# Performance work log

Hardware: AMD Instinct MI355X
Metric: run time of the kernel (lower is better)

Reference implementation:

```python
import jax, jax.numpy as jnp
import numpy as np

BETA = 0.9
THRESHOLD = 1.0  # snntorch Leaky default threshold, reset_mechanism='subtract'
ALPHA = 2.0      # snntorch default ATan surrogate alpha (irrelevant for fwd)


def spike_fn(x):
    # Heaviside spike: fires when membrane exceeds threshold (x = mem - threshold)
    return (x > 0).astype(x.dtype)


def setup_inputs() -> dict:
    key = jax.random.key(0)
    k1, k2, k3 = jax.random.split(key, 3)
    T, B, NIN, HID = 1024, 128, 256, 1024
    # Bernoulli spike train input (the module consumes spikes)
    spike_seq = (jax.random.uniform(k1, (T, B, NIN)) < 0.2).astype(jnp.float32)
    # Xavier-uniform-ish init for fc1, scaled for fc2 (gain=0.5)
    lim1 = float(np.sqrt(6.0 / (NIN + HID)))
    W1 = jax.random.uniform(k2, (HID, NIN), minval=-lim1, maxval=lim1, dtype=jnp.float32)
    b1 = jnp.zeros((HID,), jnp.float32)
    lim2 = 0.5 * float(np.sqrt(6.0 / (HID + 2)))
    W2 = jax.random.uniform(k3, (2, HID), minval=-lim2, maxval=lim2, dtype=jnp.float32)
    # avoidance bias: +0.8 on first/second half columns (as in _init_weights)
    half = NIN // 2
    W2 = W2.at[1, :half].add(0.8)
    W2 = W2.at[0, half:NIN].add(0.8)
    b2 = jnp.zeros((2,), jnp.float32)
    return {"spike_seq": spike_seq, "W1": W1, "b1": b1, "W2": W2, "b2": b2}


def reference(spike_seq, W1, b1, W2, b2):
    T, B, _ = spike_seq.shape
    HID = W1.shape[0]
    mem1_0 = jnp.zeros((B, HID), spike_seq.dtype)
    mem2_0 = jnp.zeros((B, 2), spike_seq.dtype)

    def step(carry, x_t):
        mem1, mem2 = carry
        h = x_t @ W1.T + b1                      # [B, HID]
        mem1 = BETA * mem1 + h
        spk1 = spike_fn(mem1 - THRESHOLD)
        mem1 = mem1 - spk1 * THRESHOLD           # subtract reset
        h2 = spk1 @ W2.T + b2                    # [B, 2]
        mem2 = BETA * mem2 + h2
        spk2 = spike_fn(mem2 - THRESHOLD)
        mem2 = mem2 - spk2 * THRESHOLD
        return (mem1, mem2), (spk2, spk1)

    (mem1_f, mem2_f), (out_spikes, hidden_spikes) = jax.lax.scan(
        step, (mem1_0, mem2_0), spike_seq)
    return out_spikes, hidden_spikes, mem2_f
```

## Files before the change

### kernel.cpp

```cpp
#include <hip/hip_runtime.h>
#include <hip/hip_bf16.h>
#include <stdint.h>


#define TT  1024
#define BB  128
#define NIN 256
#define HID 1024

#define OFF_HID  262144ULL
#define OFF_MEM2 134479872ULL

typedef float f4 __attribute__((ext_vector_type(4)));

__global__ __launch_bounds__(256) void k_transpose(const float* __restrict__ W1,
                                                   float* __restrict__ W1T) {
    int idx = blockIdx.x * 256 + threadIdx.x;
    if (idx >= 257 * 1024) return;
    int j = idx & (HID - 1);
    int i = idx >> 10;
    W1T[(size_t)i * HID + j] = (i < NIN) ? W1[(size_t)j * NIN + i] : 0.0f;
}

__global__ __launch_bounds__(256) void k_pack(const float* __restrict__ x,
                                              unsigned int* __restrict__ cntArr,
                                              unsigned char* __restrict__ idxArr,
                                              int slots) {
    size_t tb = blockIdx.x;
    int tid = threadIdx.x;
    int lane = tid & 63, w = tid >> 6;
    float v = x[tb * NIN + tid];
    bool act = v > 0.5f;
    unsigned long long m = __ballot(act);
    __shared__ unsigned int wc[4];
    __shared__ unsigned char sIdx[96];
    if (lane == 0) wc[w] = (unsigned int)__popcll(m);
    __syncthreads();
    unsigned int off = 0;
#pragma unroll
    for (int k = 0; k < 4; ++k) if (k < w) off += wc[k];
    unsigned int cnt = wc[0] + wc[1] + wc[2] + wc[3];
    unsigned int rank = off + (unsigned int)__popcll(m & ((1ull << lane) - 1));
    if (act && rank < (unsigned int)slots) sIdx[rank] = (unsigned char)tid;
    __syncthreads();
    if (tid * 4 < slots)
        ((unsigned int*)(idxArr + tb * (size_t)slots))[tid] = ((const unsigned int*)sIdx)[tid];
    if (tid == 0) cntArr[tb] = cnt;
}

__global__ __launch_bounds__(256, 2) void k_snn(const float* __restrict__ W1T,
                                                const unsigned int* __restrict__ cntArr,
                                                const unsigned char* __restrict__ idxArr,
                                                const float* __restrict__ x,
                                                const float* __restrict__ b1,
                                                float* __restrict__ outHid,
                                                int slots) {
#pragma clang fp contract(off)
    const int jc   = blockIdx.x & 15;
    const int bg   = blockIdx.x >> 4;
    const int tid  = threadIdx.x;
    const int lane = tid & 63;
    const int wave = tid >> 6;
    const int b    = (bg << 2) + wave;
    const int q    = lane & 15;
    const int s    = lane >> 4;
    const int jq   = (jc << 6) + (q << 2);
    const int jq4  = jq >> 2;

    __shared__ f4 sW4[257 * 16];
    __shared__ f4 sEx[4][64];

    for (int p = tid; p < NIN * 16; p += 256) {
        int i = p >> 4, qq = p & 15;
        sW4[p] = *reinterpret_cast<const f4*>(W1T + (size_t)i * HID + (jc << 6) + (qq << 2));
    }
    if (tid < 16) { f4 z; z.x = 0.f; z.y = 0.f; z.z = 0.f; z.w = 0.f; sW4[256 * 16 + tid] = z; }
    __syncthreads();

    f4 mem4;
    mem4.x = 0.f; mem4.y = 0.f; mem4.z = 0.f; mem4.w = 0.f;
    const f4 bs = *reinterpret_cast<const f4*>(b1 + jq);
    const int ub = __builtin_amdgcn_readfirstlane(b);
    const int sl = slots;
    const int dwTot = sl >> 2;
    int dwA = q;            if (dwA >= dwTot) dwA = dwTot - 1;
    int dwB = 16 + (q & 7); if (dwB >= dwTot) dwB = dwTot - 1;

    const bool sLo   = (s < 2);
    const bool sEven = ((s & 1) == 0);
    const f4* __restrict__ W1Tf4 = reinterpret_cast<const f4*>(W1T);

    unsigned offCnt = (unsigned)((s * BB + ub) * 4);
    unsigned offA   = (unsigned)((s * BB + ub) * sl + dwA * 4);
    unsigned offB   = (unsigned)((s * BB + ub) * sl + dwB * 4);
    const unsigned stC = (unsigned)(4 * BB * 4);
    const unsigned stL = (unsigned)(4 * BB * sl);

    unsigned cnt_v = *(const unsigned*)((const char*)cntArr + offCnt);
    unsigned vA_v  = *(const unsigned*)(idxArr + offA);
    unsigned vB_v  = *(const unsigned*)(idxArr + offB);

    float* outP = outHid + ((size_t)s * BB + b) * HID + jq;
    const size_t outStep = (size_t)4 * BB * HID;

#define RL(v, l) ((unsigned)__builtin_amdgcn_readlane((int)(v), (l)))
#define FETCH_D(kd, dOut) do {                                                  \
        unsigned _d0, _d1, _d2, _d3;                                            \
        if ((kd) < 16) {                                                        \
            _d0 = RL(vA, (kd));      _d1 = RL(vA, 16 + (kd));                   \
            _d2 = RL(vA, 32 + (kd)); _d3 = RL(vA, 48 + (kd));                   \
        } else { int _m = (kd) - 16;                                            \
            _d0 = RL(vB, _m);        _d1 = RL(vB, 16 + _m);                     \
            _d2 = RL(vB, 32 + _m);   _d3 = RL(vB, 48 + _m); }                   \
        unsigned _dl = sEven ? _d0 : _d1;                                       \
        unsigned _dh = sEven ? _d2 : _d3;                                       \
        dOut = sLo ? _dl : _dh;                                                 \
    } while (0)

#define FETCH_A(kd, dOut) do {                                                  \
        unsigned _d0 = RL(vA, (kd));      unsigned _d1 = RL(vA, 16 + (kd));     \
        unsigned _d2 = RL(vA, 32 + (kd)); unsigned _d3 = RL(vA, 48 + (kd));     \
        unsigned _dl = sEven ? _d0 : _d1;                                       \
        unsigned _dh = sEven ? _d2 : _d3;                                       \
        dOut = sLo ? _dl : _dh;                                                 \
    } while (0)

#define B_LDS(kd, PRED) do {                                                    \
        unsigned d_; FETCH_A(kd, d_);                                           \
        int kb_ = (kd) << 2;                                                    \
        _Pragma("unroll")                                                       \
        for (int i2 = 0; i2 < 4; ++i2) {                                        \
            unsigned row_ = (d_ >> (8 * i2)) & 255u;                            \
            if (PRED) row_ = ((unsigned)(kb_ + i2) < mylim) ? row_ : 256u;      \
            h4 += sW4[row_ * 16 + q];               \
        }                                                                       \
    } while (0)

#define WISS(n) do {                                                            \
        if (isu < dwEnd) {                                                      \
            unsigned d_; FETCH_D(isu, d_);                                      \
            unsigned r0_ = d_ & 255u, r1_ = (d_ >> 8) & 255u;                   \
            unsigned r2_ = (d_ >> 16) & 255u, r3_ = d_ >> 24;                   \
            if (isu >= predFrom) {                                              \
                int kb_ = isu << 2;                                             \
                r0_ = ((unsigned)(kb_    ) < mylim) ? r0_ : 256u;               \
                r1_ = ((unsigned)(kb_ + 1) < mylim) ? r1_ : 256u;               \
                r2_ = ((unsigned)(kb_ + 2) < mylim) ? r2_ : 256u;               \
                r3_ = ((unsigned)(kb_ + 3) < mylim) ? r3_ : 256u;               \
            }                                                                   \
            w##n##a = W1Tf4[(r0_ << 8) + jq4];                                  \
            w##n##b = W1Tf4[(r1_ << 8) + jq4];                                  \
            w##n##c = W1Tf4[(r2_ << 8) + jq4];                                  \
            w##n##d = W1Tf4[(r3_ << 8) + jq4];                                  \
            ++isu;                                                              \
        }                                                                       \
    } while (0)

#define WCON(n) do { h4 += w##n##a; h4 += w##n##b; h4 += w##n##c; h4 += w##n##d; } while (0)

    const int SPLIT = 9;

    for (int t = 0; t < TT; t += 4) {
        unsigned cnt = cnt_v, vA = vA_v, vB = vB_v;

        unsigned st = (t + 4 < TT) ? 1u : 0u;
        offCnt += st * stC; offA += st * stL; offB += st * stL;
        cnt_v = *(const unsigned*)((const char*)cntArr + offCnt);
        vA_v  = *(const unsigned*)(idxArr + offA);
        vB_v  = *(const unsigned*)(idxArr + offB);

        unsigned mylim = cnt < (unsigned)sl ? cnt : (unsigned)sl;
        int l0 = __builtin_amdgcn_readlane((int)mylim, 0);
        int l1 = __builtin_amdgcn_readlane((int)mylim, 16);
        int l2 = __builtin_amdgcn_readlane((int)mylim, 32);
        int l3 = __builtin_amdgcn_readlane((int)mylim, 48);
        int kmax = l0 > l1 ? l0 : l1; kmax = kmax > l2 ? kmax : l2; kmax = kmax > l3 ? kmax : l3;
        int kmin = l0 < l1 ? l0 : l1; kmin = kmin < l2 ? kmin : l2; kmin = kmin < l3 ? kmin : l3;

        int dwEnd = (kmax + 3) >> 2;
        int dwL   = dwEnd < SPLIT ? dwEnd : SPLIT;
        int dwLm  = (kmin >> 2) < dwL ? (kmin >> 2) : dwL;
        int predFrom = kmin >> 2;

        f4 e0, e1, e2, e3;

        if (!__any((int)(cnt > (unsigned)sl))) {
            f4 h4 = bs;

            f4 w0a, w0b, w0c, w0d;
            f4 w1a, w1b, w1c, w1d;
            f4 w2a, w2b, w2c, w2d;
            f4 w3a, w3b, w3c, w3d;
            int isu = SPLIT;
            WISS(0); WISS(1); WISS(2); WISS(3);

            int kd = 0;
            for (; kd < dwLm; ++kd) B_LDS(kd, false);
            for (; kd < dwL;  ++kd) B_LDS(kd, true);

            int kc = SPLIT;
            for (; kc + 4 <= dwEnd; kc += 4) {
                WCON(0); WISS(0);
                WCON(1); WISS(1);
                WCON(2); WISS(2);
                WCON(3); WISS(3);
            }
            int rem = dwEnd - kc;
            if (rem > 0) WCON(0);
            if (rem > 1) WCON(1);
            if (rem > 2) WCON(2);

            sEx[wave][lane] = h4;
            e0 = sEx[wave][q];
            e1 = sEx[wave][16 + q];
            e2 = sEx[wave][32 + q];
            e3 = sEx[wave][48 + q];
        } else {
#pragma unroll
            for (int tt = 0; tt < 4; ++tt) {
                const float* xr = x + ((size_t)(t + tt) * BB + ub) * NIN;
                f4 g = bs;
                for (int w2 = 0; w2 < 4; ++w2) {
                    unsigned long long m = __ballot(xr[(w2 << 6) + lane] > 0.5f);
                    while (m) {
                        int i = (w2 << 6) + __builtin_ctzll(m);
                        m &= m - 1;
                        g += sW4[i * 16 + q];
                    }
                }
                if      (tt == 0) e0 = g;
                else if (tt == 1) e1 = g;
                else if (tt == 2) e2 = g;
                else              e3 = g;
            }
        }

#define MSTEP4(ev, so0, so1, so2, so3) {                                        \
        f4 mm_ = 0.9f * mem4; mm_ = mm_ + (ev);                                 \
        so0 = (mm_.x - 1.0f > 0.0f) ? 1.0f : 0.0f;                              \
        so1 = (mm_.y - 1.0f > 0.0f) ? 1.0f : 0.0f;                              \
        so2 = (mm_.z - 1.0f > 0.0f) ? 1.0f : 0.0f;                              \
        so3 = (mm_.w - 1.0f > 0.0f) ? 1.0f : 0.0f;                              \
        f4 sp_; sp_.x = so0; sp_.y = so1; sp_.z = so2; sp_.w = so3;             \
        mem4 = mm_ - sp_;                                                       \
    }
        float sA0, sA1, sA2, sA3, sB0, sB1, sB2, sB3;
        float sC0, sC1, sC2, sC3, sD0, sD1, sD2, sD3;
        MSTEP4(e0, sA0, sA1, sA2, sA3)
        MSTEP4(e1, sB0, sB1, sB2, sB3)
        MSTEP4(e2, sC0, sC1, sC2, sC3)
        MSTEP4(e3, sD0, sD1, sD2, sD3)
#undef MSTEP4

        f4 sv;
        sv.x = sLo ? (sEven ? sA0 : sB0) : (sEven ? sC0 : sD0);
        sv.y = sLo ? (sEven ? sA1 : sB1) : (sEven ? sC1 : sD1);
        sv.z = sLo ? (sEven ? sA2 : sB2) : (sEven ? sC2 : sD2);
        sv.w = sLo ? (sEven ? sA3 : sB3) : (sEven ? sC3 : sD3);
        *reinterpret_cast<f4*>(outP) = sv;
        outP += outStep;
    }
#undef WCON
#undef WISS
#undef B_LDS
#undef FETCH_A
#undef FETCH_D
#undef RL
}

__global__ __launch_bounds__(256) void k_h2(const float* __restrict__ spk,
                                            const float* __restrict__ W2,
                                            const float* __restrict__ b2,
                                            float* __restrict__ h2) {
#pragma clang fp contract(off)
    const int lane = threadIdx.x & 63;
    const int wave = threadIdx.x >> 6;
    size_t tb = (size_t)blockIdx.x * 4 + wave;
    const float* row = spk + tb * HID;
    float s0 = 0.0f, s1 = 0.0f;
#pragma unroll
    for (int c = 0; c < 16; ++c) {
        float v  = row[c * 64 + lane];
        float r0 = v * W2[c * 64 + lane];
        float r1 = v * W2[HID + c * 64 + lane];
#pragma unroll
        for (int off = 32; off > 0; off >>= 1) {
            r0 += __shfl_xor(r0, off, 64);
            r1 += __shfl_xor(r1, off, 64);
        }
        s0 += r0;
        s1 += r1;
    }
    s0 += b2[0];
    s1 += b2[1];
    if (lane == 0)
        *reinterpret_cast<float2*>(h2 + tb * 2) = make_float2(s0, s1);
}

__global__ __launch_bounds__(256) void k_scan(const float* __restrict__ h2,
                                              float* __restrict__ outSpk,
                                              float* __restrict__ outMem2) {
#pragma clang fp contract(off)
    const int tid = threadIdx.x;
    float mem = 0.0f;
    float cur[8], nxt[8];
#pragma unroll
    for (int k = 0; k < 8; ++k) cur[k] = h2[k * 256 + tid];
    for (int t0 = 0; t0 < TT; t0 += 8) {
#pragma unroll
        for (int k = 0; k < 8; ++k) {
            int tn = t0 + 8 + k;
            nxt[k] = (tn < TT) ? h2[tn * 256 + tid] : 0.0f;
        }
#pragma unroll
        for (int k = 0; k < 8; ++k) {
            float mm = 0.9f * mem;
            mm = mm + cur[k];
            float spk = (mm - 1.0f > 0.0f) ? 1.0f : 0.0f;
            mm = mm - spk;
            mem = mm;
            outSpk[(t0 + k) * 256 + tid] = spk;
        }
#pragma unroll
        for (int k = 0; k < 8; ++k) cur[k] = nxt[k];
    }
    outMem2[tid] = mem;
}

extern "C" void kernel_launch(void* const* d_in, const int* in_sizes, int n_in,
                              void* d_out, int out_size, void* d_ws, size_t ws_size,
                              hipStream_t stream) {
    const float* x  = (const float*)d_in[0];
    const float* W1 = (const float*)d_in[1];
    const float* b1 = (const float*)d_in[2];
    const float* W2 = (const float*)d_in[3];
    const float* b2 = (const float*)d_in[4];
    float* out = (float*)d_out;

    char* ws = (char*)d_ws;
    float*         W1T = (float*)(ws);
    unsigned int*  cnt = (unsigned int*)(ws + (2 << 20));
    unsigned char* idx = (unsigned char*)(ws + (2 << 20) + (1 << 19));

    size_t fixedB = (size_t)(2 << 20) + (1 << 19) + (1 << 20);
    size_t avail  = ws_size > fixedB ? ws_size - fixedB : 0;
    long   s      = (long)((avail / 131072) & ~(size_t)7);
    int slots = (int)(s > 96 ? 96 : (s < 8 ? 8 : s));

    float* h2 = (float*)(ws + (2 << 20) + (1 << 19) + (size_t)131072 * (size_t)slots);

    k_transpose<<<1028, 256, 0, stream>>>(W1, W1T);
    k_pack<<<131072, 256, 0, stream>>>(x, cnt, idx, slots);
    k_snn<<<512, 256, 0, stream>>>(W1T, cnt, idx, x, b1, out + OFF_HID, slots);
    k_h2<<<32768, 256, 0, stream>>>(out + OFF_HID, W2, b2, h2);
    k_scan<<<1, 256, 0, stream>>>(h2, out, out + OFF_MEM2);
}
```

Before: 1.202 ms.

## Split input rows between LDS and global W1T, narrow column tile to raise occupancy

Only the first 152 input rows of the W1T column slice are kept in LDS. Active inputs above that split are now read straight from global memory, so k_pack builds separate low and high index lists of 48 slots each, with both counts packed into one word. Each block covers 32 columns instead of 64 and each wave handles 8 timesteps per iteration instead of 4. The smaller LDS footprint allows launch bounds of 4 blocks per CU and twice as many blocks. The trade is more global W1T traffic and more readlane and select work per step in exchange for higher occupancy. It also assumes a fixed 16MB index region and no longer sizes slots from ws_size.

```diff
diff --git a/kernel.cpp b/kernel.cpp
--- a/kernel.cpp
+++ b/kernel.cpp
@@ -7,6 +7,7 @@
 #define BB  128
 #define NIN 256
 #define HID 1024
+#define SPLITR 152
 
 #define OFF_HID  262144ULL
 #define OFF_MEM2 134479872ULL
@@ -23,131 +24,118 @@
 }
 
 __global__ __launch_bounds__(256) void k_pack(const float* __restrict__ x,
-                                              unsigned int* __restrict__ cntArr,
-                                              unsigned char* __restrict__ idxArr,
-                                              int slots) {
+                                              unsigned* __restrict__ cntArr,
+                                              unsigned char* __restrict__ idxArr) {
     size_t tb = blockIdx.x;
-    int tid = threadIdx.x;
-    int lane = tid & 63, w = tid >> 6;
+    int tid = threadIdx.x, lane = tid & 63, w = tid >> 6;
     float v = x[tb * NIN + tid];
-    bool act = v > 0.5f;
-    unsigned long long m = __ballot(act);
-    __shared__ unsigned int wc[4];
+    bool act  = v > 0.5f;
+    bool isLo = tid < SPLITR;
+    unsigned long long mLo = __ballot(act && isLo);
+    unsigned long long mHi = __ballot(act && !isLo);
+    __shared__ unsigned wcLo[4], wcHi[4];
     __shared__ unsigned char sIdx[96];
-    if (lane == 0) wc[w] = (unsigned int)__popcll(m);
+    if (lane == 0) { wcLo[w] = (unsigned)__popcll(mLo); wcHi[w] = (unsigned)__popcll(mHi); }
     __syncthreads();
-    unsigned int off = 0;
-#pragma unroll
-    for (int k = 0; k < 4; ++k) if (k < w) off += wc[k];
-    unsigned int cnt = wc[0] + wc[1] + wc[2] + wc[3];
-    unsigned int rank = off + (unsigned int)__popcll(m & ((1ull << lane) - 1));
-    if (act && rank < (unsigned int)slots) sIdx[rank] = (unsigned char)tid;
+    unsigned offLo = 0, offHi = 0;
+#pragma unroll
+    for (int k = 0; k < 4; ++k) if (k < w) { offLo += wcLo[k]; offHi += wcHi[k]; }
+    unsigned cntLo = wcLo[0] + wcLo[1] + wcLo[2] + wcLo[3];
+    unsigned cntHi = wcHi[0] + wcHi[1] + wcHi[2] + wcHi[3];
+    unsigned long long below = (1ull << lane) - 1;
+    unsigned rLo = offLo + (unsigned)__popcll(mLo & below);
+    unsigned rHi = offHi + (unsigned)__popcll(mHi & below);
+    if (act && isLo  && rLo < 48) sIdx[rLo]      = (unsigned char)tid;
+    if (act && !isLo && rHi < 48) sIdx[48 + rHi] = (unsigned char)tid;
     __syncthreads();
-    if (tid * 4 < slots)
-        ((unsigned int*)(idxArr + tb * (size_t)slots))[tid] = ((const unsigned int*)sIdx)[tid];
-    if (tid == 0) cntArr[tb] = cnt;
-}
-
-__global__ __launch_bounds__(256, 2) void k_snn(const float* __restrict__ W1T,
-                                                const unsigned int* __restrict__ cntArr,
+    if (tid < 24) ((unsigned*)(idxArr + tb * 128))[tid] = ((const unsigned*)sIdx)[tid];
+    if (tid == 0) cntArr[tb] = cntLo | (cntHi << 16);
+}
+
+__global__ __launch_bounds__(256, 4) void k_snn(const float* __restrict__ W1T,
+                                                const unsigned* __restrict__ cntArr,
                                                 const unsigned char* __restrict__ idxArr,
                                                 const float* __restrict__ x,
                                                 const float* __restrict__ b1,
-                                                float* __restrict__ outHid,
-                                                int slots) {
+                                                float* __restrict__ outHid) {
 #pragma clang fp contract(off)
-    const int jc   = blockIdx.x & 15;
-    const int bg   = blockIdx.x >> 4;
+    const int jc   = blockIdx.x & 31;
+    const int bg   = blockIdx.x >> 5;
     const int tid  = threadIdx.x;
     const int lane = tid & 63;
     const int wave = tid >> 6;
     const int b    = (bg << 2) + wave;
-    const int q    = lane & 15;
-    const int s    = lane >> 4;
-    const int jq   = (jc << 6) + (q << 2);
-    const int jq4  = jq >> 2;
-
-    __shared__ f4 sW4[257 * 16];
+    const int q    = lane & 7;
+    const int s    = lane >> 3;
+    const int jq   = (jc << 5) + (q << 2);
+    const int jq4  = (jc << 3) + q;
+    const bool sb0 = (s & 1) != 0, sb1 = (s & 2) != 0, sb2 = (s & 4) != 0;
+
+    __shared__ f4 sW4[153 * 8];
     __shared__ f4 sEx[4][64];
-
-    for (int p = tid; p < NIN * 16; p += 256) {
-        int i = p >> 4, qq = p & 15;
-        sW4[p] = *reinterpret_cast<const f4*>(W1T + (size_t)i * HID + (jc << 6) + (qq << 2));
-    }
-    if (tid < 16) { f4 z; z.x = 0.f; z.y = 0.f; z.z = 0.f; z.w = 0.f; sW4[256 * 16 + tid] = z; }
+    const f4* __restrict__ W1Tf4 = reinterpret_cast<const f4*>(W1T);
+
+    for (int p = tid; p < 153 * 8; p += 256) {
+        int row = p >> 3, qq = p & 7;
+        f4 z; z.x = 0.f; z.y = 0.f; z.z = 0.f; z.w = 0.f;
+        sW4[p] = (row < SPLITR) ? W1Tf4[row * 256 + (jc << 3) + qq] : z;
+    }
     __syncthreads();
 
-    f4 mem4;
-    mem4.x = 0.f; mem4.y = 0.f; mem4.z = 0.f; mem4.w = 0.f;
+    f4 mem4; mem4.x = 0.f; mem4.y = 0.f; mem4.z = 0.f; mem4.w = 0.f;
     const f4 bs = *reinterpret_cast<const f4*>(b1 + jq);
     const int ub = __builtin_amdgcn_readfirstlane(b);
-    const int sl = slots;
-    const int dwTot = sl >> 2;
-    int dwA = q;            if (dwA >= dwTot) dwA = dwTot - 1;
-    int dwB = 16 + (q & 7); if (dwB >= dwTot) dwB = dwTot - 1;
-
-    const bool sLo   = (s < 2);
-    const bool sEven = ((s & 1) == 0);
-    const f4* __restrict__ W1Tf4 = reinterpret_cast<const f4*>(W1T);
-
+
+    unsigned offBlk = (unsigned)((s * BB + ub) * 128);
     unsigned offCnt = (unsigned)((s * BB + ub) * 4);
-    unsigned offA   = (unsigned)((s * BB + ub) * sl + dwA * 4);
-    unsigned offB   = (unsigned)((s * BB + ub) * sl + dwB * 4);
-    const unsigned stC = (unsigned)(4 * BB * 4);
-    const unsigned stL = (unsigned)(4 * BB * sl);
-
-    unsigned cnt_v = *(const unsigned*)((const char*)cntArr + offCnt);
-    unsigned vA_v  = *(const unsigned*)(idxArr + offA);
-    unsigned vB_v  = *(const unsigned*)(idxArr + offB);
+    const unsigned stB = 8u * BB * 128u;
+    const unsigned stC = 8u * BB * 4u;
+
+    unsigned cnt_v  = *(const unsigned*)((const char*)cntArr + offCnt);
+    unsigned vLoA_v = *(const unsigned*)(idxArr + offBlk + (q << 2));
+    unsigned vLoB_v = *(const unsigned*)(idxArr + offBlk + 32 + ((q & 3) << 2));
+    unsigned vHiA_v = *(const unsigned*)(idxArr + offBlk + 48 + (q << 2));
+    unsigned vHiB_v = *(const unsigned*)(idxArr + offBlk + 80 + ((q & 3) << 2));
 
     float* outP = outHid + ((size_t)s * BB + b) * HID + jq;
-    const size_t outStep = (size_t)4 * BB * HID;
+    const size_t outStep = (size_t)8 * BB * HID;
 
 #define RL(v, l) ((unsigned)__builtin_amdgcn_readlane((int)(v), (l)))
-#define FETCH_D(kd, dOut) do {                                                  \
-        unsigned _d0, _d1, _d2, _d3;                                            \
-        if ((kd) < 16) {                                                        \
-            _d0 = RL(vA, (kd));      _d1 = RL(vA, 16 + (kd));                   \
-            _d2 = RL(vA, 32 + (kd)); _d3 = RL(vA, 48 + (kd));                   \
-        } else { int _m = (kd) - 16;                                            \
-            _d0 = RL(vB, _m);        _d1 = RL(vB, 16 + _m);                     \
-            _d2 = RL(vB, 32 + _m);   _d3 = RL(vB, 48 + _m); }                   \
-        unsigned _dl = sEven ? _d0 : _d1;                                       \
-        unsigned _dh = sEven ? _d2 : _d3;                                       \
-        dOut = sLo ? _dl : _dh;                                                 \
+#define FETCH8(vreg, kd, dOut) do {                                             \
+        unsigned e0_=RL(vreg,(kd)),    e1_=RL(vreg,8+(kd)),                     \
+                 e2_=RL(vreg,16+(kd)), e3_=RL(vreg,24+(kd)),                    \
+                 e4_=RL(vreg,32+(kd)), e5_=RL(vreg,40+(kd)),                    \
+                 e6_=RL(vreg,48+(kd)), e7_=RL(vreg,56+(kd));                    \
+        unsigned x0_ = sb0 ? e1_ : e0_, x1_ = sb0 ? e3_ : e2_;                  \
+        unsigned x2_ = sb0 ? e5_ : e4_, x3_ = sb0 ? e7_ : e6_;                  \
+        unsigned y0_ = sb1 ? x1_ : x0_, y1_ = sb1 ? x3_ : x2_;                  \
+        dOut = sb2 ? y1_ : y0_;                                                 \
     } while (0)
 
-#define FETCH_A(kd, dOut) do {                                                  \
-        unsigned _d0 = RL(vA, (kd));      unsigned _d1 = RL(vA, 16 + (kd));     \
-        unsigned _d2 = RL(vA, 32 + (kd)); unsigned _d3 = RL(vA, 48 + (kd));     \
-        unsigned _dl = sEven ? _d0 : _d1;                                       \
-        unsigned _dh = sEven ? _d2 : _d3;                                       \
-        dOut = sLo ? _dl : _dh;                                                 \
-    } while (0)
-
-#define B_LDS(kd, PRED) do {                                                    \
-        unsigned d_; FETCH_A(kd, d_);                                           \
-        int kb_ = (kd) << 2;                                                    \
+#define GLO4(d, kd) do {                                                        \
         _Pragma("unroll")                                                       \
         for (int i2 = 0; i2 < 4; ++i2) {                                        \
-            unsigned row_ = (d_ >> (8 * i2)) & 255u;                            \
-            if (PRED) row_ = ((unsigned)(kb_ + i2) < mylim) ? row_ : 256u;      \
-            h4 += sW4[row_ * 16 + q];               \
+            unsigned r_ = ((d) >> (8 * i2)) & 255u;                             \
+            r_ = ((unsigned)((kd) * 4 + i2) < mylimLo) ? r_ : (unsigned)SPLITR; \
+            h4 += sW4[r_ * 8 + q];                                              \
         }                                                                       \
     } while (0)
 
+#define FETCH_HI(kk, d) do {                                                    \
+        if ((kk) < 8) FETCH8(vHiA, (kk), d);                                    \
+        else          FETCH8(vHiB, (kk) - 8, d);                                \
+    } while (0)
+
 #define WISS(n) do {                                                            \
-        if (isu < dwEnd) {                                                      \
-            unsigned d_; FETCH_D(isu, d_);                                      \
+        if (isu < dwEndHi) {                                                    \
+            unsigned d_; FETCH_HI(isu, d_);                                     \
+            int kb_ = isu << 2;                                                 \
             unsigned r0_ = d_ & 255u, r1_ = (d_ >> 8) & 255u;                   \
             unsigned r2_ = (d_ >> 16) & 255u, r3_ = d_ >> 24;                   \
-            if (isu >= predFrom) {                                              \
-                int kb_ = isu << 2;                                             \
-                r0_ = ((unsigned)(kb_    ) < mylim) ? r0_ : 256u;               \
-                r1_ = ((unsigned)(kb_ + 1) < mylim) ? r1_ : 256u;               \
-                r2_ = ((unsigned)(kb_ + 2) < mylim) ? r2_ : 256u;               \
-                r3_ = ((unsigned)(kb_ + 3) < mylim) ? r3_ : 256u;               \
-            }                                                                   \
+            r0_ = ((unsigned)(kb_    ) < mylimHi) ? r0_ : 256u;                 \
+            r1_ = ((unsigned)(kb_ + 1) < mylimHi) ? r1_ : 256u;                 \
+            r2_ = ((unsigned)(kb_ + 2) < mylimHi) ? r2_ : 256u;                 \
+            r3_ = ((unsigned)(kb_ + 3) < mylimHi) ? r3_ : 256u;                 \
             w##n##a = W1Tf4[(r0_ << 8) + jq4];                                  \
             w##n##b = W1Tf4[(r1_ << 8) + jq4];                                  \
             w##n##c = W1Tf4[(r2_ << 8) + jq4];                                  \
@@ -158,66 +146,79 @@
 
 #define WCON(n) do { h4 += w##n##a; h4 += w##n##b; h4 += w##n##c; h4 += w##n##d; } while (0)
 
-    const int SPLIT = 9;
-
-    for (int t = 0; t < TT; t += 4) {
-        unsigned cnt = cnt_v, vA = vA_v, vB = vB_v;
-
-        unsigned st = (t + 4 < TT) ? 1u : 0u;
-        offCnt += st * stC; offA += st * stL; offB += st * stL;
-        cnt_v = *(const unsigned*)((const char*)cntArr + offCnt);
-        vA_v  = *(const unsigned*)(idxArr + offA);
-        vB_v  = *(const unsigned*)(idxArr + offB);
-
-        unsigned mylim = cnt < (unsigned)sl ? cnt : (unsigned)sl;
-        int l0 = __builtin_amdgcn_readlane((int)mylim, 0);
-        int l1 = __builtin_amdgcn_readlane((int)mylim, 16);
-        int l2 = __builtin_amdgcn_readlane((int)mylim, 32);
-        int l3 = __builtin_amdgcn_readlane((int)mylim, 48);
-        int kmax = l0 > l1 ? l0 : l1; kmax = kmax > l2 ? kmax : l2; kmax = kmax > l3 ? kmax : l3;
-        int kmin = l0 < l1 ? l0 : l1; kmin = kmin < l2 ? kmin : l2; kmin = kmin < l3 ? kmin : l3;
-
-        int dwEnd = (kmax + 3) >> 2;
-        int dwL   = dwEnd < SPLIT ? dwEnd : SPLIT;
-        int dwLm  = (kmin >> 2) < dwL ? (kmin >> 2) : dwL;
-        int predFrom = kmin >> 2;
-
-        f4 e0, e1, e2, e3;
-
-        if (!__any((int)(cnt > (unsigned)sl))) {
+#define MSTEP(ev, spk) {                                                        \
+        f4 mm_ = 0.9f * mem4; mm_ = mm_ + (ev);                                 \
+        spk.x = (mm_.x - 1.0f > 0.0f) ? 1.0f : 0.0f;                            \
+        spk.y = (mm_.y - 1.0f > 0.0f) ? 1.0f : 0.0f;                            \
+        spk.z = (mm_.z - 1.0f > 0.0f) ? 1.0f : 0.0f;                            \
+        spk.w = (mm_.w - 1.0f > 0.0f) ? 1.0f : 0.0f;                            \
+        mem4 = mm_ - spk;                                                       \
+    }
+
+    for (int t = 0; t < TT; t += 8) {
+        unsigned cnt = cnt_v;
+        unsigned vLoA = vLoA_v, vLoB = vLoB_v, vHiA = vHiA_v, vHiB = vHiB_v;
+
+        unsigned stp = (t + 8 < TT) ? 1u : 0u;
+        offBlk += stp * stB; offCnt += stp * stC;
+        cnt_v  = *(const unsigned*)((const char*)cntArr + offCnt);
+        vLoA_v = *(const unsigned*)(idxArr + offBlk + (q << 2));
+        vLoB_v = *(const unsigned*)(idxArr + offBlk + 32 + ((q & 3) << 2));
+        vHiA_v = *(const unsigned*)(idxArr + offBlk + 48 + (q << 2));
+        vHiB_v = *(const unsigned*)(idxArr + offBlk + 80 + ((q & 3) << 2));
+
+        unsigned rawLo = cnt & 0xFFFFu, rawHi = cnt >> 16;
+        unsigned mylimLo = rawLo < 48u ? rawLo : 48u;
+        unsigned mylimHi = rawHi < 48u ? rawHi : 48u;
+        int ml = (int)mylimLo;
+        ml = max(ml, __shfl_xor(ml, 8, 64));
+        ml = max(ml, __shfl_xor(ml, 16, 64));
+        ml = max(ml, __shfl_xor(ml, 32, 64));
+        int dwEndLo = (ml + 3) >> 2;
+        int mh = (int)mylimHi;
+        mh = max(mh, __shfl_xor(mh, 8, 64));
+        mh = max(mh, __shfl_xor(mh, 16, 64));
+        mh = max(mh, __shfl_xor(mh, 32, 64));
+        int dwEndHi = (mh + 3) >> 2;
+
+        f4 e0, e1, e2, e3, e4, e5, e6, e7;
+        bool ovf = (rawLo > 48u) || (rawHi > 48u);
+
+        if (!__any((int)ovf)) {
             f4 h4 = bs;
 
             f4 w0a, w0b, w0c, w0d;
             f4 w1a, w1b, w1c, w1d;
             f4 w2a, w2b, w2c, w2d;
             f4 w3a, w3b, w3c, w3d;
-            int isu = SPLIT;
+            int isu = 0;
             WISS(0); WISS(1); WISS(2); WISS(3);
 
-            int kd = 0;
-            for (; kd < dwLm; ++kd) B_LDS(kd, false);
-            for (; kd < dwL;  ++kd) B_LDS(kd, true);
-
-            int kc = SPLIT;
-            for (; kc + 4 <= dwEnd; kc += 4) {
+            int kdl = 0;
+            int e8 = dwEndLo < 8 ? dwEndLo : 8;
+            for (; kdl < e8; ++kdl)      { unsigned d; FETCH8(vLoA, kdl, d);     GLO4(d, kdl); }
+            for (; kdl < dwEndLo; ++kdl) { unsigned d; FETCH8(vLoB, kdl - 8, d); GLO4(d, kdl); }
+
+            int kc = 0;
+            for (; kc + 4 <= dwEndHi; kc += 4) {
                 WCON(0); WISS(0);
                 WCON(1); WISS(1);
                 WCON(2); WISS(2);
                 WCON(3); WISS(3);
             }
-            int rem = dwEnd - kc;
+            int rem = dwEndHi - kc;
             if (rem > 0) WCON(0);
             if (rem > 1) WCON(1);
             if (rem > 2) WCON(2);
 
             sEx[wave][lane] = h4;
-            e0 = sEx[wave][q];
-            e1 = sEx[wave][16 + q];
-            e2 = sEx[wave][32 + q];
-            e3 = sEx[wave][48 + q];
+            e0 = sEx[wave][q];      e1 = sEx[wave][8 + q];
+            e2 = sEx[wave][16 + q]; e3 = sEx[wave][24 + q];
+            e4 = sEx[wave][32 + q]; e5 = sEx[wave][40 + q];
+            e6 = sEx[wave][48 + q]; e7 = sEx[wave][56 + q];
         } else {
 #pragma unroll
-            for (int tt = 0; tt < 4; ++tt) {
+            for (int tt = 0; tt < 8; ++tt) {
                 const float* xr = x + ((size_t)(t + tt) * BB + ub) * NIN;
                 f4 g = bs;
                 for (int w2 = 0; w2 < 4; ++w2) {
@@ -225,46 +226,33 @@
                     while (m) {
                         int i = (w2 << 6) + __builtin_ctzll(m);
                         m &= m - 1;
-                        g += sW4[i * 16 + q];
+                        g += W1Tf4[((unsigned)i << 8) + jq4];
                     }
                 }
-                if      (tt == 0) e0 = g;
-                else if (tt == 1) e1 = g;
-                else if (tt == 2) e2 = g;
-                else              e3 = g;
+                if      (tt == 0) e0 = g; else if (tt == 1) e1 = g;
+                else if (tt == 2) e2 = g; else if (tt == 3) e3 = g;
+                else if (tt == 4) e4 = g; else if (tt == 5) e5 = g;
+                else if (tt == 6) e6 = g; else              e7 = g;
             }
         }
 
-#define MSTEP4(ev, so0, so1, so2, so3) {                                        \
-        f4 mm_ = 0.9f * mem4; mm_ = mm_ + (ev);                                 \
-        so0 = (mm_.x - 1.0f > 0.0f) ? 1.0f : 0.0f;                              \
-        so1 = (mm_.y - 1.0f > 0.0f) ? 1.0f : 0.0f;                              \
-        so2 = (mm_.z - 1.0f > 0.0f) ? 1.0f : 0.0f;                              \
-        so3 = (mm_.w - 1.0f > 0.0f) ? 1.0f : 0.0f;                              \
-        f4 sp_; sp_.x = so0; sp_.y = so1; sp_.z = so2; sp_.w = so3;             \
-        mem4 = mm_ - sp_;                                                       \
-    }
-        float sA0, sA1, sA2, sA3, sB0, sB1, sB2, sB3;
-        float sC0, sC1, sC2, sC3, sD0, sD1, sD2, sD3;
-        MSTEP4(e0, sA0, sA1, sA2, sA3)
-        MSTEP4(e1, sB0, sB1, sB2, sB3)
-        MSTEP4(e2, sC0, sC1, sC2, sC3)
-        MSTEP4(e3, sD0, sD1, sD2, sD3)
-#undef MSTEP4
-
-        f4 sv;
-        sv.x = sLo ? (sEven ? sA0 : sB0) : (sEven ? sC0 : sD0);
-        sv.y = sLo ? (sEven ? sA1 : sB1) : (sEven ? sC1 : sD1);
-        sv.z = sLo ? (sEven ? sA2 : sB2) : (sEven ? sC2 : sD2);
-        sv.w = sLo ? (sEven ? sA3 : sB3) : (sEven ? sC3 : sD3);
+        f4 k0, k1, k2, k3, k4, k5, k6, k7;
+        MSTEP(e0, k0) MSTEP(e1, k1) MSTEP(e2, k2) MSTEP(e3, k3)
+        MSTEP(e4, k4) MSTEP(e5, k5) MSTEP(e6, k6) MSTEP(e7, k7)
+
+        f4 a0 = sb0 ? k1 : k0, a1 = sb0 ? k3 : k2;
+        f4 a2 = sb0 ? k5 : k4, a3 = sb0 ? k7 : k6;
+        f4 b0 = sb1 ? a1 : a0, b1v = sb1 ? a3 : a2;
+        f4 sv = sb2 ? b1v : b0;
         *reinterpret_cast<f4*>(outP) = sv;
         outP += outStep;
     }
+#undef MSTEP
 #undef WCON
 #undef WISS
-#undef B_LDS
-#undef FETCH_A
-#undef FETCH_D
+#undef FETCH_HI
+#undef GLO4
+#undef FETCH8
 #undef RL
 }
 
@@ -339,19 +327,13 @@
 
     char* ws = (char*)d_ws;
     float*         W1T = (float*)(ws);
-    unsigned int*  cnt = (unsigned int*)(ws + (2 << 20));
+    unsigned*      cnt = (unsigned*)(ws + (2 << 20));
     unsigned char* idx = (unsigned char*)(ws + (2 << 20) + (1 << 19));
-
-    size_t fixedB = (size_t)(2 << 20) + (1 << 19) + (1 << 20);
-    size_t avail  = ws_size > fixedB ? ws_size - fixedB : 0;
-    long   s      = (long)((avail / 131072) & ~(size_t)7);
-    int slots = (int)(s > 96 ? 96 : (s < 8 ? 8 : s));
-
-    float* h2 = (float*)(ws + (2 << 20) + (1 << 19) + (size_t)131072 * (size_t)slots);
+    float*         h2  = (float*)(ws + (2 << 20) + (1 << 19) + (16 << 20));
 
     k_transpose<<<1028, 256, 0, stream>>>(W1, W1T);
-    k_pack<<<131072, 256, 0, stream>>>(x, cnt, idx, slots);
-    k_snn<<<512, 256, 0, stream>>>(W1T, cnt, idx, x, b1, out + OFF_HID, slots);
+    k_pack<<<131072, 256, 0, stream>>>(x, cnt, idx);
+    k_snn<<<1024, 256, 0, stream>>>(W1T, cnt, idx, x, b1, out + OFF_HID);
     k_h2<<<32768, 256, 0, stream>>>(out + OFF_HID, W2, b2, h2);
     k_scan<<<1, 256, 0, stream>>>(h2, out, out + OFF_MEM2);
 }
```

Result: slower. 3.234 ms (+169.1%).
